# Performance work log

Hardware: AMD Instinct MI355X
Metric: run time of the kernel (lower is better)

The kernel has to match this reference:

```python
import jax, jax.numpy as jnp
import numpy as np


def setup_inputs() -> dict:
    key = jax.random.key(0)
    k1, k2, k3, k4 = jax.random.split(key, 4)
    B, T, C, H = 8, 2048, 1024, 1024
    return {
        "x": jax.random.normal(k1, (B, T, C), dtype=jnp.float32),
        "Wk": jax.random.normal(k2, (H, C), dtype=jnp.float32),
        "Wq": jax.random.normal(k3, (H, C), dtype=jnp.float32),
        "Wv": jax.random.normal(k4, (H, C), dtype=jnp.float32),
    }


def reference(x, Wk, Wq, Wv):
    # x: [B, T, C]; Wk/Wq/Wv: [H, C] (torch Linear stores [fan_out, fan_in])
    B, T, C = x.shape
    k = jnp.einsum('btc,hc->bth', x, Wk)  # [B, T, H]
    q = jnp.einsum('btc,hc->bth', x, Wq)
    v = jnp.einsum('btc,hc->bth', x, Wv)
    # NOTE: source scales by n_embd (C) ** -0.5, not head_size
    wei = jnp.einsum('bth,bsh->bts', q, k) * (C ** -0.5)  # [B, T, T]
    causal = jnp.tril(jnp.ones((T, T), dtype=bool))
    wei = jnp.where(causal, wei, -jnp.inf)
    wei = jax.nn.softmax(wei, axis=-1)
    # Dropout omitted (inference behavior; p=0.5 train-only in source)
    out = jnp.einsum('bts,bsh->bth', wei, v)  # [B, T, H]
    return (out, wei)
```

## Files before the change

kernel.cpp:

```cpp
#include <hip/hip_runtime.h>
#include <hip/hip_bf16.h>


#define BB 8
#define TT 2048
#define CC 1024
#define HH 1024
#define BT (BB * TT)

typedef _Float16 f16x8 __attribute__((ext_vector_type(8)));
typedef _Float16 f16x4 __attribute__((ext_vector_type(4)));
typedef float f32x4 __attribute__((ext_vector_type(4)));

#define AS1 __attribute__((address_space(1)))
#define AS3 __attribute__((address_space(3)))

__device__ __forceinline__ void gld16(const _Float16* g, _Float16* lds) {
    __builtin_amdgcn_global_load_lds((AS1 const unsigned int*)g,
                                     (AS3 unsigned int*)lds, 16, 0, 0);
}

__global__ __launch_bounds__(256) void split_kernel(
    const float* __restrict__ src, _Float16* __restrict__ dh,
    _Float16* __restrict__ dl, int n)
{
    int i = (blockIdx.x * 256 + threadIdx.x) * 4;
    if (i >= n) return;
    float4 v = *(const float4*)(src + i);
    f16x4 h, l;
    h[0] = (_Float16)v.x; l[0] = (_Float16)(v.x - (float)h[0]);
    h[1] = (_Float16)v.y; l[1] = (_Float16)(v.y - (float)h[1]);
    h[2] = (_Float16)v.z; l[2] = (_Float16)(v.z - (float)h[2]);
    h[3] = (_Float16)v.w; l[3] = (_Float16)(v.w - (float)h[3]);
    *(f16x4*)&dh[i] = h;
    *(f16x4*)&dl[i] = l;
}

__global__ __launch_bounds__(256) void splitT_kernel(
    const float* __restrict__ W, _Float16* __restrict__ th,
    _Float16* __restrict__ tl)
{
    __shared__ float L[64][65];
    const int h0 = blockIdx.x * 64;
    const int c0 = blockIdx.y * 64;
    const int tid = threadIdx.x;
    {
        const int hl = tid >> 2;
        const int cs = (tid & 3) * 16;
#pragma unroll
        for (int jj = 0; jj < 16; jj += 4) {
            float4 v = *(const float4*)&W[(size_t)(h0 + hl) * CC + c0 + cs + jj];
            L[cs + jj + 0][hl] = v.x;
            L[cs + jj + 1][hl] = v.y;
            L[cs + jj + 2][hl] = v.z;
            L[cs + jj + 3][hl] = v.w;
        }
    }
    __syncthreads();
    const int c  = tid >> 2;
    const int hs = (tid & 3) * 16;
    f16x8 hv0, hv1, lv0, lv1;
#pragma unroll
    for (int i = 0; i < 8; ++i) {
        float a = L[c][hs + i], b = L[c][hs + 8 + i];
        hv0[i] = (_Float16)a; lv0[i] = (_Float16)(a - (float)hv0[i]);
        hv1[i] = (_Float16)b; lv1[i] = (_Float16)(b - (float)hv1[i]);
    }
    size_t o = (size_t)(c0 + c) * HH + h0 + hs;
    *(f16x8*)&th[o] = hv0; *(f16x8*)&th[o + 8] = hv1;
    *(f16x8*)&tl[o] = lv0; *(f16x8*)&tl[o + 8] = lv1;
}

__global__ __launch_bounds__(256, 2) void mm_kernel(
    const _Float16* __restrict__ aH, const _Float16* __restrict__ aL,
    const _Float16* __restrict__ bH, const _Float16* __restrict__ bL,
    _Float16* __restrict__ mtH, _Float16* __restrict__ mtL)
{
    __shared__ _Float16 Ah[4096], Al[4096], Bh[4096], Bl[4096];

    const int n0 = blockIdx.x * 128;
    const int m0 = blockIdx.y * 128;

    const int tid  = threadIdx.x;
    const int r0   = tid & 127;
    const int k0   = tid >> 7;
    const int wave = tid >> 6;
    const int lane = tid & 63;
    const int quad = lane >> 4;
    const int lrow = lane & 15;
    const int wr   = (wave >> 1) * 64;
    const int wc   = (wave & 1) * 64;

    const size_t ga = (size_t)(m0 + r0) * HH + k0 * 8;
    const size_t gb = (size_t)(n0 + r0) * HH + k0 * 8;
    const int lds0 = tid * 8, lds1 = (tid + 256) * 8;

    f32x4 acc[4][4] = {};

    for (int kc = 0; kc < HH; kc += 32) {
        __syncthreads();
        gld16(aH + ga + kc,      &Ah[lds0]);
        gld16(aH + ga + kc + 16, &Ah[lds1]);
        gld16(aL + ga + kc,      &Al[lds0]);
        gld16(aL + ga + kc + 16, &Al[lds1]);
        gld16(bH + gb + kc,      &Bh[lds0]);
        gld16(bH + gb + kc + 16, &Bh[lds1]);
        gld16(bL + gb + kc,      &Bl[lds0]);
        gld16(bL + gb + kc + 16, &Bl[lds1]);
        __syncthreads();

        f16x8 ahf[4], alf[4], bhf[4], blf[4];
#pragma unroll
        for (int i = 0; i < 4; ++i) {
            ahf[i] = *(const f16x8*)&Ah[(quad * 128 + wr + i * 16 + lrow) * 8];
            alf[i] = *(const f16x8*)&Al[(quad * 128 + wr + i * 16 + lrow) * 8];
            bhf[i] = *(const f16x8*)&Bh[(quad * 128 + wc + i * 16 + lrow) * 8];
            blf[i] = *(const f16x8*)&Bl[(quad * 128 + wc + i * 16 + lrow) * 8];
        }
#pragma unroll
        for (int i = 0; i < 4; ++i)
#pragma unroll
            for (int j = 0; j < 4; ++j) {
                acc[i][j] = __builtin_amdgcn_mfma_f32_16x16x32_f16(ahf[i], bhf[j], acc[i][j], 0, 0, 0);
                acc[i][j] = __builtin_amdgcn_mfma_f32_16x16x32_f16(ahf[i], blf[j], acc[i][j], 0, 0, 0);
                acc[i][j] = __builtin_amdgcn_mfma_f32_16x16x32_f16(alf[i], bhf[j], acc[i][j], 0, 0, 0);
            }
    }

#pragma unroll
    for (int i = 0; i < 4; ++i)
#pragma unroll
        for (int j = 0; j < 4; ++j) {
            int mm = m0 + wr + i * 16 + quad * 4;
            int nn = n0 + wc + j * 16 + lrow;
            f16x4 ph, pl;
#pragma unroll
            for (int r = 0; r < 4; ++r) {
                float val = acc[i][j][r];
                _Float16 h = (_Float16)val;
                ph[r] = h;
                pl[r] = (_Float16)(val - (float)h);
            }
            *(f16x4*)&mtH[(size_t)nn * CC + mm] = ph;
            *(f16x4*)&mtL[(size_t)nn * CC + mm] = pl;
        }
}

#define EPI_STRIDE 136
__global__ __launch_bounds__(256, 2) void pv_kernel(
    const _Float16* __restrict__ xh, const _Float16* __restrict__ xl,
    const _Float16* __restrict__ mtH, const _Float16* __restrict__ mtL,
    const _Float16* __restrict__ Wvh,
    _Float16* __restrict__ Ph, _Float16* __restrict__ Pl,
    _Float16* __restrict__ vT)
{
    __shared__ _Float16 S[24576];

    const int idx   = blockIdx.x;
    const int z     = idx >> 10;
    const int r     = idx & 1023;
    const int xcd   = r & 7;
    const int j7    = r >> 3;
    const int mtile = xcd * 16 + (j7 >> 3);
    const int ntile = j7 & 7;
    const int m0 = mtile * 128;
    const int n0 = ntile * 128;

    const int tid  = threadIdx.x;
    const int r0   = tid & 127;
    const int k0   = tid >> 7;
    const int wave = tid >> 6;
    const int lane = tid & 63;
    const int quad = lane >> 4;
    const int lrow = lane & 15;
    const int wr   = (wave >> 1) * 64;
    const int wc   = (wave & 1) * 64;

    const size_t ga = (size_t)(m0 + r0) * CC + k0 * 8;
    const int lds0 = tid * 8, lds1 = (tid + 256) * 8;

    f32x4 acc[4][4] = {};

    if (z == 0) {
#define PV_A(kc_, sp_) do { \
        _Float16* Sb = S + (sp_) * 8192; \
        gld16(xh + ga + (kc_),      &Sb[lds0]); \
        gld16(xh + ga + (kc_) + 16, &Sb[lds1]); \
        gld16(xl + ga + (kc_),      &Sb[4096 + lds0]); \
        gld16(xl + ga + (kc_) + 16, &Sb[4096 + lds1]); \
    } while (0)
        PV_A(0, 0);
        PV_A(32, 1);
        int sa = 0;
        for (int kc = 0; kc < CC; kc += 32) {
            asm volatile("s_waitcnt vmcnt(4)" ::: "memory");
            __builtin_amdgcn_s_barrier();
            __builtin_amdgcn_sched_barrier(0);

            f16x8 bhf[4], blf[4];
#pragma unroll
            for (int j = 0; j < 4; ++j) {
                const size_t gbj = (size_t)(n0 + wc + j * 16 + lrow) * CC + kc + quad * 8;
                bhf[j] = *(const f16x8*)&mtH[gbj];
                blf[j] = *(const f16x8*)&mtL[gbj];
            }
            __builtin_amdgcn_sched_barrier(0);

            int ka = kc + 64; if (ka > CC - 32) ka = CC - 32;
            int s2 = sa + 2; if (s2 >= 3) s2 -= 3;
            PV_A(ka, s2);
            __builtin_amdgcn_sched_barrier(0);

            const _Float16* Ah = S + sa * 8192;
            const _Float16* Al = Ah + 4096;
            f16x8 ahf[4], alf[4];
#pragma unroll
            for (int i = 0; i < 4; ++i) {
                ahf[i] = *(const f16x8*)&Ah[(quad * 128 + wr + i * 16 + lrow) * 8];
                alf[i] = *(const f16x8*)&Al[(quad * 128 + wr + i * 16 + lrow) * 8];
            }
            __builtin_amdgcn_s_setprio(1);
#pragma unroll
            for (int i = 0; i < 4; ++i)
#pragma unroll
                for (int j = 0; j < 4; ++j) {
                    acc[i][j] = __builtin_amdgcn_mfma_f32_16x16x32_f16(ahf[i], bhf[j], acc[i][j], 0, 0, 0);
                    acc[i][j] = __builtin_amdgcn_mfma_f32_16x16x32_f16(ahf[i], blf[j], acc[i][j], 0, 0, 0);
                    acc[i][j] = __builtin_amdgcn_mfma_f32_16x16x32_f16(alf[i], bhf[j], acc[i][j], 0, 0, 0);
                }
            __builtin_amdgcn_s_setprio(0);

            ++sa; if (sa == 3) sa = 0;
        }
    } else {
#define PV_S1(kc_, sp_) do { \
        _Float16* Sb = S + (sp_) * 4096; \
        gld16(xh + ga + (kc_),      &Sb[lds0]); \
        gld16(xh + ga + (kc_) + 16, &Sb[lds1]); \
    } while (0)
        PV_S1(0, 0);
        PV_S1(32, 1);
        int sl = 0;
        for (int kc = 0; kc < CC; kc += 32) {
            asm volatile("s_waitcnt vmcnt(2)" ::: "memory");
            __builtin_amdgcn_s_barrier();
            __builtin_amdgcn_sched_barrier(0);

            f16x8 bhf[4];
#pragma unroll
            for (int j = 0; j < 4; ++j) {
                const size_t gbj = (size_t)(n0 + wc + j * 16 + lrow) * CC + kc + quad * 8;
                bhf[j] = *(const f16x8*)&Wvh[gbj];
            }
            __builtin_amdgcn_sched_barrier(0);

            int ka = kc + 64; if (ka > CC - 32) ka = CC - 32;
            int s2 = sl + 2; if (s2 >= 3) s2 -= 3;
            PV_S1(ka, s2);
            __builtin_amdgcn_sched_barrier(0);

            const _Float16* Ah = S + sl * 4096;
            f16x8 ahf[4];
#pragma unroll
            for (int i = 0; i < 4; ++i)
                ahf[i] = *(const f16x8*)&Ah[(quad * 128 + wr + i * 16 + lrow) * 8];
            __builtin_amdgcn_s_setprio(1);
#pragma unroll
            for (int i = 0; i < 4; ++i)
#pragma unroll
                for (int j = 0; j < 4; ++j)
                    acc[i][j] = __builtin_amdgcn_mfma_f32_16x16x32_f16(ahf[i], bhf[j], acc[i][j], 0, 0, 0);
            __builtin_amdgcn_s_setprio(0);

            ++sl; if (sl == 3) sl = 0;
        }
    }

    asm volatile("s_waitcnt vmcnt(0)" ::: "memory");
    __syncthreads();

    if (z == 1) {
#pragma unroll
        for (int i = 0; i < 4; ++i)
#pragma unroll
            for (int j = 0; j < 4; ++j) {
                int hl = wc + j * 16 + lrow;
                int tl = wr + i * 16 + quad * 4;
                f16x4 p;
#pragma unroll
                for (int rr = 0; rr < 4; ++rr) p[rr] = (_Float16)acc[i][j][rr];
                *(f16x4*)&S[hl * EPI_STRIDE + tl] = p;
            }
        __syncthreads();
        const int bi  = mtile >> 4;
        const int t0g = (mtile & 15) * 128;
        _Float16* vb = vT + (size_t)bi * HH * TT;
#pragma unroll
        for (int rr = 0; rr < 128; rr += 16) {
            int h = rr + (tid >> 4);
            int t = (tid & 15) * 8;
            f16x8 val = *(const f16x8*)&S[h * EPI_STRIDE + t];
            *(f16x8*)&vb[(size_t)(n0 + h) * TT + t0g + t] = val;
        }
    } else {
#pragma unroll
        for (int i = 0; i < 4; ++i)
#pragma unroll
            for (int j = 0; j < 4; ++j) {
                int tl = wr + i * 16 + quad * 4;
                int cl = wc + j * 16 + lrow;
#pragma unroll
                for (int rr = 0; rr < 4; ++rr)
                    S[(tl + rr) * EPI_STRIDE + cl] = (_Float16)acc[i][j][rr];
            }
        __syncthreads();
#pragma unroll
        for (int rr = 0; rr < 128; rr += 16) {
            int t = rr + (tid >> 4);
            int c = (tid & 15) * 8;
            f16x8 val = *(const f16x8*)&S[t * EPI_STRIDE + c];
            *(f16x8*)&Ph[(size_t)(m0 + t) * CC + n0 + c] = val;
        }
        __syncthreads();
#pragma unroll
        for (int i = 0; i < 4; ++i)
#pragma unroll
            for (int j = 0; j < 4; ++j) {
                int tl = wr + i * 16 + quad * 4;
                int cl = wc + j * 16 + lrow;
#pragma unroll
                for (int rr = 0; rr < 4; ++rr) {
                    float val = acc[i][j][rr];
                    _Float16 h = (_Float16)val;
                    S[(tl + rr) * EPI_STRIDE + cl] = (_Float16)(val - (float)h);
                }
            }
        __syncthreads();
#pragma unroll
        for (int rr = 0; rr < 128; rr += 16) {
            int t = rr + (tid >> 4);
            int c = (tid & 15) * 8;
            f16x8 val = *(const f16x8*)&S[t * EPI_STRIDE + c];
            *(f16x8*)&Pl[(size_t)(m0 + t) * CC + n0 + c] = val;
        }
    }
}

__global__ __launch_bounds__(256, 2) void logits_kernel(
    const _Float16* __restrict__ Ph, const _Float16* __restrict__ Pl,
    const _Float16* __restrict__ xh, const _Float16* __restrict__ xl,
    float* __restrict__ wei)
{
    __shared__ _Float16 S[24576];

    const int id  = blockIdx.x;
    const int b   = id & 7;
    const int tri = id >> 3;
    int tt = (int)((sqrtf(8.0f * (float)tri + 1.0f) - 1.0f) * 0.5f);
    while ((tt + 1) * (tt + 2) / 2 <= tri) ++tt;
    while (tt * (tt + 1) / 2 > tri) --tt;
    const int st = tri - tt * (tt + 1) / 2;

    const size_t base = (size_t)b * TT * CC;
    float* wb = wei + (size_t)b * TT * TT;
    const int m0 = tt * 128;
    const int n0 = st * 128;

    const int tid  = threadIdx.x;
    const int r0   = tid & 127;
    const int k0   = tid >> 7;
    const int wave = tid >> 6;
    const int lane = tid & 63;
    const int quad = lane >> 4;
    const int lrow = lane & 15;
    const int wr   = (wave >> 1) * 64;
    const int wc   = (wave & 1) * 64;

    const size_t ga = base + (size_t)(m0 + r0) * CC + k0 * 8;
    const _Float16* xhb = xh + base;
    const _Float16* xlb = xl + base;
    const int lds0 = tid * 8, lds1 = (tid + 256) * 8;

    f32x4 acc[4][4] = {};

#define LG_A(kc_, sp_) do { \
    _Float16* Sb = S + (sp_) * 8192; \
    gld16(Ph + ga + (kc_),      &Sb[lds0]); \
    gld16(Ph + ga + (kc_) + 16, &Sb[lds1]); \
    gld16(Pl + ga + (kc_),      &Sb[4096 + lds0]); \
    gld16(Pl + ga + (kc_) + 16, &Sb[4096 + lds1]); \
} while (0)

    LG_A(0, 0);
    LG_A(32, 1);

    int sa = 0;
    for (int kc = 0; kc < CC; kc += 32) {
        asm volatile("s_waitcnt vmcnt(4)" ::: "memory");
        __builtin_amdgcn_s_barrier();
        __builtin_amdgcn_sched_barrier(0);

        f16x8 bhf[4], blf[4];
#pragma unroll
        for (int j = 0; j < 4; ++j) {
            const size_t gbj = (size_t)(n0 + wc + j * 16 + lrow) * CC + kc + quad * 8;
            bhf[j] = *(const f16x8*)&xhb[gbj];
            blf[j] = *(const f16x8*)&xlb[gbj];
        }
        __builtin_amdgcn_sched_barrier(0);

        int ka = kc + 64; if (ka > CC - 32) ka = CC - 32;
        int s2 = sa + 2; if (s2 >= 3) s2 -= 3;
        LG_A(ka, s2);
        __builtin_amdgcn_sched_barrier(0);

        const _Float16* Ah = S + sa * 8192;
        const _Float16* Al = Ah + 4096;
        f16x8 ahf[4], alf[4];
#pragma unroll
        for (int i = 0; i < 4; ++i) {
            ahf[i] = *(const f16x8*)&Ah[(quad * 128 + wr + i * 16 + lrow) * 8];
            alf[i] = *(const f16x8*)&Al[(quad * 128 + wr + i * 16 + lrow) * 8];
        }
        __builtin_amdgcn_s_setprio(1);
#pragma unroll
        for (int i = 0; i < 4; ++i)
#pragma unroll
            for (int j = 0; j < 4; ++j) {
                acc[i][j] = __builtin_amdgcn_mfma_f32_16x16x32_f16(ahf[i], bhf[j], acc[i][j], 0, 0, 0);
                acc[i][j] = __builtin_amdgcn_mfma_f32_16x16x32_f16(ahf[i], blf[j], acc[i][j], 0, 0, 0);
                acc[i][j] = __builtin_amdgcn_mfma_f32_16x16x32_f16(alf[i], bhf[j], acc[i][j], 0, 0, 0);
            }
        __builtin_amdgcn_s_setprio(0);

        ++sa; if (sa == 3) sa = 0;
    }

    asm volatile("s_waitcnt vmcnt(0)" ::: "memory");

    const float scale = 0.03125f;
#pragma unroll
    for (int i = 0; i < 4; ++i)
#pragma unroll
        for (int j = 0; j < 4; ++j)
#pragma unroll
            for (int r = 0; r < 4; ++r) {
                int rr = wr + i * 16 + quad * 4 + r;
                int cc = wc + j * 16 + lrow;
                wb[(size_t)(m0 + rr) * TT + n0 + cc] = acc[i][j][r] * scale;
            }
}

__global__ __launch_bounds__(256) void softmax_kernel(
    float* __restrict__ wei, _Float16* __restrict__ wei16)
{
    const int t = blockIdx.x;
    const int b = blockIdx.y;
    float* row = wei + (size_t)b * TT * TT + (size_t)t * TT;
    _Float16* row16 = wei16 + (size_t)b * TT * TT + (size_t)t * TT;
    const int n = t + 1;
    const int tid = threadIdx.x;
    const int base = tid * 8;

    float vals[8];
    if (base < n) {
        float4 v0 = *(const float4*)&row[base];
        float4 v1 = *(const float4*)&row[base + 4];
        vals[0] = v0.x; vals[1] = v0.y; vals[2] = v0.z; vals[3] = v0.w;
        vals[4] = v1.x; vals[5] = v1.y; vals[6] = v1.z; vals[7] = v1.w;
    } else {
#pragma unroll
        for (int i = 0; i < 8; ++i) vals[i] = -INFINITY;
    }

    float mx = -INFINITY;
#pragma unroll
    for (int i = 0; i < 8; ++i) {
        if (base + i >= n) vals[i] = -INFINITY;
        mx = fmaxf(mx, vals[i]);
    }
#pragma unroll
    for (int off = 32; off > 0; off >>= 1)
        mx = fmaxf(mx, __shfl_down(mx, off));

    __shared__ float redm[4];
    __shared__ float reds[4];
    if ((tid & 63) == 0) redm[tid >> 6] = mx;
    __syncthreads();
    const float m = fmaxf(fmaxf(redm[0], redm[1]), fmaxf(redm[2], redm[3]));

    float sum = 0.f;
#pragma unroll
    for (int i = 0; i < 8; ++i) {
        vals[i] = __expf(vals[i] - m);
        sum += vals[i];
    }
#pragma unroll
    for (int off = 32; off > 0; off >>= 1)
        sum += __shfl_down(sum, off);
    if ((tid & 63) == 0) reds[tid >> 6] = sum;
    __syncthreads();
    const float inv = 1.0f / (reds[0] + reds[1] + reds[2] + reds[3]);

    f16x8 h;
#pragma unroll
    for (int i = 0; i < 8; ++i) {
        float w = vals[i] * inv;
        vals[i] = w;
        h[i] = (_Float16)w;
    }
    *(float4*)&row[base]     = make_float4(vals[0], vals[1], vals[2], vals[3]);
    *(float4*)&row[base + 4] = make_float4(vals[4], vals[5], vals[6], vals[7]);
    *(f16x8*)&row16[base]    = h;
}

__global__ __launch_bounds__(256, 3) void out_kernel(
    const _Float16* __restrict__ wei16, const _Float16* __restrict__ vT,
    float* __restrict__ out)
{
    __shared__ _Float16 S[12288];

    const int id = blockIdx.x;
    const int b  = id & 7;
    const int r  = id >> 3;
    const int tt = 15 - (r >> 3);
    const int nb = r & 7;

    const _Float16* wb = wei16 + (size_t)b * TT * TT;
    const _Float16* vb = vT    + (size_t)b * HH * TT;
    float*          ob = out   + (size_t)b * TT * HH;

    const int m0 = tt * 128;
    const int n0 = nb * 128;
    const int kend = (tt + 1) * 128;

    const int tid  = threadIdx.x;
    const int r0   = tid & 127;
    const int k0   = tid >> 7;
    const int wave = tid >> 6;
    const int lane = tid & 63;
    const int quad = lane >> 4;
    const int lrow = lane & 15;
    const int wr   = (wave >> 1) * 64;
    const int wc   = (wave & 1) * 64;

    const size_t ga = (size_t)(m0 + r0) * TT + k0 * 8;
    const int lds0 = tid * 8, lds1 = (tid + 256) * 8;

    f32x4 acc[4][4] = {};

#define OUT_A(kc_, sp_) do { \
    _Float16* Sb = S + (sp_) * 4096; \
    gld16(wb + ga + (kc_),      &Sb[lds0]); \
    gld16(wb + ga + (kc_) + 16, &Sb[lds1]); \
} while (0)

    OUT_A(0, 0);
    OUT_A(32, 1);

    int sl = 0;
    for (int kc = 0; kc < kend; kc += 32) {
        asm volatile("s_waitcnt vmcnt(2)" ::: "memory");
        __builtin_amdgcn_s_barrier();
        __builtin_amdgcn_sched_barrier(0);

        f16x8 bhf[4];
#pragma unroll
        for (int j = 0; j < 4; ++j) {
            const size_t gbj = (size_t)(n0 + wc + j * 16 + lrow) * TT + kc + quad * 8;
            bhf[j] = *(const f16x8*)&vb[gbj];
        }
        __builtin_amdgcn_sched_barrier(0);

        int ka = kc + 64; if (ka > kend - 32) ka = kend - 32;
        int s2 = sl + 2; if (s2 >= 3) s2 -= 3;
        OUT_A(ka, s2);
        __builtin_amdgcn_sched_barrier(0);

        const _Float16* Ah = S + sl * 4096;
        f16x8 ahf[4];
#pragma unroll
        for (int i = 0; i < 4; ++i)
            ahf[i] = *(const f16x8*)&Ah[(quad * 128 + wr + i * 16 + lrow) * 8];
        __builtin_amdgcn_s_setprio(1);
#pragma unroll
        for (int i = 0; i < 4; ++i)
#pragma unroll
            for (int j = 0; j < 4; ++j)
                acc[i][j] = __builtin_amdgcn_mfma_f32_16x16x32_f16(ahf[i], bhf[j], acc[i][j], 0, 0, 0);
        __builtin_amdgcn_s_setprio(0);

        ++sl; if (sl == 3) sl = 0;
    }

    asm volatile("s_waitcnt vmcnt(0)" ::: "memory");

#pragma unroll
    for (int i = 0; i < 4; ++i)
#pragma unroll
        for (int j = 0; j < 4; ++j)
#pragma unroll
            for (int r2 = 0; r2 < 4; ++r2) {
                int rr = wr + i * 16 + quad * 4 + r2;
                int cc = wc + j * 16 + lrow;
                ob[(size_t)(m0 + rr) * HH + n0 + cc] = acc[i][j][r2];
            }
}

extern "C" void kernel_launch(void* const* d_in, const int* in_sizes, int n_in,
                              void* d_out, int out_size, void* d_ws, size_t ws_size,
                              hipStream_t stream)
{
    const float* x  = (const float*)d_in[0];
    const float* Wk = (const float*)d_in[1];
    const float* Wq = (const float*)d_in[2];
    const float* Wv = (const float*)d_in[3];

    const size_t NX = (size_t)BT * CC;
    const size_t NW = (size_t)HH * CC;

    float* out = (float*)d_out;
    float* wei = out + (size_t)BT * HH;

    _Float16* WqTh = (_Float16*)out;
    _Float16* WqTl = WqTh + NW;
    _Float16* WkTh = WqTl + NW;
    _Float16* WkTl = WkTh + NW;
    _Float16* Wvh  = WkTl + NW;
    _Float16* Wvl  = Wvh  + NW;
    _Float16* MTh  = Wvl  + NW;
    _Float16* MTl  = MTh  + NW;

    _Float16* xh = (_Float16*)d_ws;
    _Float16* xl = xh + NX;
    _Float16* Ph = xl + NX;
    _Float16* Pl = Ph + NX;
    _Float16* vT = Pl + NX;
    _Float16* wei16 = (_Float16*)d_ws;

    split_kernel<<<dim3(NX / 1024), 256, 0, stream>>>(x, xh, xl, (int)NX);
    splitT_kernel<<<dim3(HH / 64, CC / 64), 256, 0, stream>>>(Wq, WqTh, WqTl);
    splitT_kernel<<<dim3(HH / 64, CC / 64), 256, 0, stream>>>(Wk, WkTh, WkTl);
    split_kernel<<<dim3(NW / 1024), 256, 0, stream>>>(Wv, Wvh, Wvl, (int)NW);

    mm_kernel<<<dim3(CC / 128, CC / 128), 256, 0, stream>>>(
        WqTh, WqTl, WkTh, WkTl, MTh, MTl);
    pv_kernel<<<dim3(2048), 256, 0, stream>>>(
        xh, xl, MTh, MTl, Wvh, Ph, Pl, vT);
    logits_kernel<<<dim3(136 * BB), 256, 0, stream>>>(
        Ph, Pl, xh, xl, wei);
    softmax_kernel<<<dim3(TT, BB), 256, 0, stream>>>(wei, wei16);
    out_kernel<<<dim3(128 * BB), 256, 0, stream>>>(wei16, vT, out);
}
```

Baseline: 967.3 us.

## Prefetch B-operand register fragments one k-step ahead in the GEMM loops

The three MFMA GEMM loops (projection, QK^T logits, and PV output) now load the next k-slice's B-operand fragments from global memory into a second register set while the current slice is computed. The loop is unrolled by two to ping-pong between the two register sets. This hides global-load latency that was previously exposed right after the barrier. In exchange it uses more VGPRs, drops the s_setprio hints, and assumes the output loop's k extent is a multiple of 64.

```diff
diff --git a/kernel.cpp b/kernel.cpp
--- a/kernel.cpp
+++ b/kernel.cpp
@@ -189,90 +189,105 @@
         gld16(xl + ga + (kc_),      &Sb[4096 + lds0]); \
         gld16(xl + ga + (kc_) + 16, &Sb[4096 + lds1]); \
     } while (0)
+
+#define PV_ITER0(kc_, BHC, BLC, BHN, BLN) do { \
+        asm volatile("s_waitcnt vmcnt(4)" ::: "memory"); \
+        __builtin_amdgcn_s_barrier(); \
+        __builtin_amdgcn_sched_barrier(0); \
+        { int kb = (kc_) + 32; if (kb > CC - 32) kb = CC - 32; \
+          _Pragma("unroll") \
+          for (int j = 0; j < 4; ++j) { \
+              const size_t gbj = (size_t)(n0 + wc + j * 16 + lrow) * CC + kb + quad * 8; \
+              BHN[j] = *(const f16x8*)&mtH[gbj]; \
+              BLN[j] = *(const f16x8*)&mtL[gbj]; \
+          } } \
+        __builtin_amdgcn_sched_barrier(0); \
+        { int ka = (kc_) + 64; if (ka > CC - 32) ka = CC - 32; \
+          int s2 = sa + 2; if (s2 >= 3) s2 -= 3; \
+          PV_A(ka, s2); } \
+        __builtin_amdgcn_sched_barrier(0); \
+        { const _Float16* Ah = S + sa * 8192; \
+          const _Float16* Al = Ah + 4096; \
+          f16x8 ahf[4], alf[4]; \
+          _Pragma("unroll") \
+          for (int i = 0; i < 4; ++i) { \
+              ahf[i] = *(const f16x8*)&Ah[(quad * 128 + wr + i * 16 + lrow) * 8]; \
+              alf[i] = *(const f16x8*)&Al[(quad * 128 + wr + i * 16 + lrow) * 8]; \
+          } \
+          _Pragma("unroll") \
+          for (int i = 0; i < 4; ++i) \
+              _Pragma("unroll") \
+              for (int j = 0; j < 4; ++j) { \
+                  acc[i][j] = __builtin_amdgcn_mfma_f32_16x16x32_f16(ahf[i], BHC[j], acc[i][j], 0, 0, 0); \
+                  acc[i][j] = __builtin_amdgcn_mfma_f32_16x16x32_f16(ahf[i], BLC[j], acc[i][j], 0, 0, 0); \
+                  acc[i][j] = __builtin_amdgcn_mfma_f32_16x16x32_f16(alf[i], BHC[j], acc[i][j], 0, 0, 0); \
+              } } \
+        ++sa; if (sa == 3) sa = 0; \
+    } while (0)
+
+        f16x8 bhA[4], blA[4], bhB[4], blB[4];
+#pragma unroll
+        for (int j = 0; j < 4; ++j) {
+            const size_t gbj = (size_t)(n0 + wc + j * 16 + lrow) * CC + quad * 8;
+            bhA[j] = *(const f16x8*)&mtH[gbj];
+            blA[j] = *(const f16x8*)&mtL[gbj];
+        }
+        __builtin_amdgcn_sched_barrier(0);
         PV_A(0, 0);
         PV_A(32, 1);
         int sa = 0;
-        for (int kc = 0; kc < CC; kc += 32) {
-            asm volatile("s_waitcnt vmcnt(4)" ::: "memory");
-            __builtin_amdgcn_s_barrier();
-            __builtin_amdgcn_sched_barrier(0);
-
-            f16x8 bhf[4], blf[4];
-#pragma unroll
-            for (int j = 0; j < 4; ++j) {
-                const size_t gbj = (size_t)(n0 + wc + j * 16 + lrow) * CC + kc + quad * 8;
-                bhf[j] = *(const f16x8*)&mtH[gbj];
-                blf[j] = *(const f16x8*)&mtL[gbj];
-            }
-            __builtin_amdgcn_sched_barrier(0);
-
-            int ka = kc + 64; if (ka > CC - 32) ka = CC - 32;
-            int s2 = sa + 2; if (s2 >= 3) s2 -= 3;
-            PV_A(ka, s2);
-            __builtin_amdgcn_sched_barrier(0);
-
-            const _Float16* Ah = S + sa * 8192;
-            const _Float16* Al = Ah + 4096;
-            f16x8 ahf[4], alf[4];
-#pragma unroll
-            for (int i = 0; i < 4; ++i) {
-                ahf[i] = *(const f16x8*)&Ah[(quad * 128 + wr + i * 16 + lrow) * 8];
-                alf[i] = *(const f16x8*)&Al[(quad * 128 + wr + i * 16 + lrow) * 8];
-            }
-            __builtin_amdgcn_s_setprio(1);
-#pragma unroll
-            for (int i = 0; i < 4; ++i)
-#pragma unroll
-                for (int j = 0; j < 4; ++j) {
-                    acc[i][j] = __builtin_amdgcn_mfma_f32_16x16x32_f16(ahf[i], bhf[j], acc[i][j], 0, 0, 0);
-                    acc[i][j] = __builtin_amdgcn_mfma_f32_16x16x32_f16(ahf[i], blf[j], acc[i][j], 0, 0, 0);
-                    acc[i][j] = __builtin_amdgcn_mfma_f32_16x16x32_f16(alf[i], bhf[j], acc[i][j], 0, 0, 0);
-                }
-            __builtin_amdgcn_s_setprio(0);
-
-            ++sa; if (sa == 3) sa = 0;
+        for (int kc = 0; kc < CC; kc += 64) {
+            PV_ITER0(kc,      bhA, blA, bhB, blB);
+            PV_ITER0(kc + 32, bhB, blB, bhA, blA);
         }
     } else {
-#define PV_S1(kc_, sp_) do { \
+#define PV_A1(kc_, sp_) do { \
         _Float16* Sb = S + (sp_) * 4096; \
         gld16(xh + ga + (kc_),      &Sb[lds0]); \
         gld16(xh + ga + (kc_) + 16, &Sb[lds1]); \
     } while (0)
-        PV_S1(0, 0);
-        PV_S1(32, 1);
+
+#define PV_ITER1(kc_, BHC, BHN) do { \
+        asm volatile("s_waitcnt vmcnt(2)" ::: "memory"); \
+        __builtin_amdgcn_s_barrier(); \
+        __builtin_amdgcn_sched_barrier(0); \
+        { int kb = (kc_) + 32; if (kb > CC - 32) kb = CC - 32; \
+          _Pragma("unroll") \
+          for (int j = 0; j < 4; ++j) { \
+              const size_t gbj = (size_t)(n0 + wc + j * 16 + lrow) * CC + kb + quad * 8; \
+              BHN[j] = *(const f16x8*)&Wvh[gbj]; \
+          } } \
+        __builtin_amdgcn_sched_barrier(0); \
+        { int ka = (kc_) + 64; if (ka > CC - 32) ka = CC - 32; \
+          int s2 = sl + 2; if (s2 >= 3) s2 -= 3; \
+          PV_A1(ka, s2); } \
+        __builtin_amdgcn_sched_barrier(0); \
+        { const _Float16* Ah = S + sl * 4096; \
+          f16x8 ahf[4]; \
+          _Pragma("unroll") \
+          for (int i = 0; i < 4; ++i) \
+              ahf[i] = *(const f16x8*)&Ah[(quad * 128 + wr + i * 16 + lrow) * 8]; \
+          _Pragma("unroll") \
+          for (int i = 0; i < 4; ++i) \
+              _Pragma("unroll") \
+              for (int j = 0; j < 4; ++j) \
+                  acc[i][j] = __builtin_amdgcn_mfma_f32_16x16x32_f16(ahf[i], BHC[j], acc[i][j], 0, 0, 0); } \
+        ++sl; if (sl == 3) sl = 0; \
+    } while (0)
+
+        f16x8 bhA[4], bhB[4];
+#pragma unroll
+        for (int j = 0; j < 4; ++j) {
+            const size_t gbj = (size_t)(n0 + wc + j * 16 + lrow) * CC + quad * 8;
+            bhA[j] = *(const f16x8*)&Wvh[gbj];
+        }
+        __builtin_amdgcn_sched_barrier(0);
+        PV_A1(0, 0);
+        PV_A1(32, 1);
         int sl = 0;
-        for (int kc = 0; kc < CC; kc += 32) {
-            asm volatile("s_waitcnt vmcnt(2)" ::: "memory");
-            __builtin_amdgcn_s_barrier();
-            __builtin_amdgcn_sched_barrier(0);
-
-            f16x8 bhf[4];
-#pragma unroll
-            for (int j = 0; j < 4; ++j) {
-                const size_t gbj = (size_t)(n0 + wc + j * 16 + lrow) * CC + kc + quad * 8;
-                bhf[j] = *(const f16x8*)&Wvh[gbj];
-            }
-            __builtin_amdgcn_sched_barrier(0);
-
-            int ka = kc + 64; if (ka > CC - 32) ka = CC - 32;
-            int s2 = sl + 2; if (s2 >= 3) s2 -= 3;
-            PV_S1(ka, s2);
-            __builtin_amdgcn_sched_barrier(0);
-
-            const _Float16* Ah = S + sl * 4096;
-            f16x8 ahf[4];
-#pragma unroll
-            for (int i = 0; i < 4; ++i)
-                ahf[i] = *(const f16x8*)&Ah[(quad * 128 + wr + i * 16 + lrow) * 8];
-            __builtin_amdgcn_s_setprio(1);
-#pragma unroll
-            for (int i = 0; i < 4; ++i)
-#pragma unroll
-                for (int j = 0; j < 4; ++j)
-                    acc[i][j] = __builtin_amdgcn_mfma_f32_16x16x32_f16(ahf[i], bhf[j], acc[i][j], 0, 0, 0);
-            __builtin_amdgcn_s_setprio(0);
-
-            ++sl; if (sl == 3) sl = 0;
+        for (int kc = 0; kc < CC; kc += 64) {
+            PV_ITER1(kc,      bhA, bhB);
+            PV_ITER1(kc + 32, bhB, bhA);
         }
     }
 
@@ -391,49 +406,55 @@
     gld16(Pl + ga + (kc_) + 16, &Sb[4096 + lds1]); \
 } while (0)
 
+#define LG_ITER(kc_, BHC, BLC, BHN, BLN) do { \
+    asm volatile("s_waitcnt vmcnt(4)" ::: "memory"); \
+    __builtin_amdgcn_s_barrier(); \
+    __builtin_amdgcn_sched_barrier(0); \
+    { int kb = (kc_) + 32; if (kb > CC - 32) kb = CC - 32; \
+      _Pragma("unroll") \
+      for (int j = 0; j < 4; ++j) { \
+          const size_t gbj = (size_t)(n0 + wc + j * 16 + lrow) * CC + kb + quad * 8; \
+          BHN[j] = *(const f16x8*)&xhb[gbj]; \
+          BLN[j] = *(const f16x8*)&xlb[gbj]; \
+      } } \
+    __builtin_amdgcn_sched_barrier(0); \
+    { int ka = (kc_) + 64; if (ka > CC - 32) ka = CC - 32; \
+      int s2 = sa + 2; if (s2 >= 3) s2 -= 3; \
+      LG_A(ka, s2); } \
+    __builtin_amdgcn_sched_barrier(0); \
+    { const _Float16* Ah = S + sa * 8192; \
+      const _Float16* Al = Ah + 4096; \
+      f16x8 ahf[4], alf[4]; \
+      _Pragma("unroll") \
+      for (int i = 0; i < 4; ++i) { \
+          ahf[i] = *(const f16x8*)&Ah[(quad * 128 + wr + i * 16 + lrow) * 8]; \
+          alf[i] = *(const f16x8*)&Al[(quad * 128 + wr + i * 16 + lrow) * 8]; \
+      } \
+      _Pragma("unroll") \
+      for (int i = 0; i < 4; ++i) \
+          _Pragma("unroll") \
+          for (int j = 0; j < 4; ++j) { \
+              acc[i][j] = __builtin_amdgcn_mfma_f32_16x16x32_f16(ahf[i], BHC[j], acc[i][j], 0, 0, 0); \
+              acc[i][j] = __builtin_amdgcn_mfma_f32_16x16x32_f16(ahf[i], BLC[j], acc[i][j], 0, 0, 0); \
+              acc[i][j] = __builtin_amdgcn_mfma_f32_16x16x32_f16(alf[i], BHC[j], acc[i][j], 0, 0, 0); \
+          } } \
+    ++sa; if (sa == 3) sa = 0; \
+} while (0)
+
+    f16x8 bhA[4], blA[4], bhB[4], blB[4];
+#pragma unroll
+    for (int j = 0; j < 4; ++j) {
+        const size_t gbj = (size_t)(n0 + wc + j * 16 + lrow) * CC + quad * 8;
+        bhA[j] = *(const f16x8*)&xhb[gbj];
+        blA[j] = *(const f16x8*)&xlb[gbj];
+    }
+    __builtin_amdgcn_sched_barrier(0);
     LG_A(0, 0);
     LG_A(32, 1);
-
     int sa = 0;
-    for (int kc = 0; kc < CC; kc += 32) {
-        asm volatile("s_waitcnt vmcnt(4)" ::: "memory");
-        __builtin_amdgcn_s_barrier();
-        __builtin_amdgcn_sched_barrier(0);
-
-        f16x8 bhf[4], blf[4];
-#pragma unroll
-        for (int j = 0; j < 4; ++j) {
-            const size_t gbj = (size_t)(n0 + wc + j * 16 + lrow) * CC + kc + quad * 8;
-            bhf[j] = *(const f16x8*)&xhb[gbj];
-            blf[j] = *(const f16x8*)&xlb[gbj];
-        }
-        __builtin_amdgcn_sched_barrier(0);
-
-        int ka = kc + 64; if (ka > CC - 32) ka = CC - 32;
-        int s2 = sa + 2; if (s2 >= 3) s2 -= 3;
-        LG_A(ka, s2);
-        __builtin_amdgcn_sched_barrier(0);
-
-        const _Float16* Ah = S + sa * 8192;
-        const _Float16* Al = Ah + 4096;
-        f16x8 ahf[4], alf[4];
-#pragma unroll
-        for (int i = 0; i < 4; ++i) {
-            ahf[i] = *(const f16x8*)&Ah[(quad * 128 + wr + i * 16 + lrow) * 8];
-            alf[i] = *(const f16x8*)&Al[(quad * 128 + wr + i * 16 + lrow) * 8];
-        }
-        __builtin_amdgcn_s_setprio(1);
-#pragma unroll
-        for (int i = 0; i < 4; ++i)
-#pragma unroll
-            for (int j = 0; j < 4; ++j) {
-                acc[i][j] = __builtin_amdgcn_mfma_f32_16x16x32_f16(ahf[i], bhf[j], acc[i][j], 0, 0, 0);
-                acc[i][j] = __builtin_amdgcn_mfma_f32_16x16x32_f16(ahf[i], blf[j], acc[i][j], 0, 0, 0);
-                acc[i][j] = __builtin_amdgcn_mfma_f32_16x16x32_f16(alf[i], bhf[j], acc[i][j], 0, 0, 0);
-            }
-        __builtin_amdgcn_s_setprio(0);
-
-        ++sa; if (sa == 3) sa = 0;
+    for (int kc = 0; kc < CC; kc += 64) {
+        LG_ITER(kc,      bhA, blA, bhB, blB);
+        LG_ITER(kc + 32, bhB, blB, bhA, blA);
     }
 
     asm volatile("s_waitcnt vmcnt(0)" ::: "memory");
@@ -555,42 +576,45 @@
     gld16(wb + ga + (kc_) + 16, &Sb[lds1]); \
 } while (0)
 
+#define OUT_ITER(kc_, BHC, BHN) do { \
+    asm volatile("s_waitcnt vmcnt(2)" ::: "memory"); \
+    __builtin_amdgcn_s_barrier(); \
+    __builtin_amdgcn_sched_barrier(0); \
+    { int kb = (kc_) + 32; if (kb > kend - 32) kb = kend - 32; \
+      _Pragma("unroll") \
+      for (int j = 0; j < 4; ++j) { \
+          const size_t gbj = (size_t)(n0 + wc + j * 16 + lrow) * TT + kb + quad * 8; \
+          BHN[j] = *(const f16x8*)&vb[gbj]; \
+      } } \
+    __builtin_amdgcn_sched_barrier(0); \
+    { int ka = (kc_) + 64; if (ka > kend - 32) ka = kend - 32; \
+      int s2 = sl + 2; if (s2 >= 3) s2 -= 3; \
+      OUT_A(ka, s2); } \
+    __builtin_amdgcn_sched_barrier(0); \
+    { const _Float16* Ah = S + sl * 4096; \
+      f16x8 ahf[4]; \
+      _Pragma("unroll") \
+      for (int i = 0; i < 4; ++i) \
+          ahf[i] = *(const f16x8*)&Ah[(quad * 128 + wr + i * 16 + lrow) * 8]; \
+      _Pragma("unroll") \
+      for (int i = 0; i < 4; ++i) \
+          _Pragma("unroll") \
+          for (int j = 0; j < 4; ++j) \
+              acc[i][j] = __builtin_amdgcn_mfma_f32_16x16x32_f16(ahf[i], BHC[j], acc[i][j], 0, 0, 0); } \
+    ++sl; if (sl == 3) sl = 0; \
+} while (0)
+
+    f16x8 bvA[4], bvB[4];
+#pragma unroll
+    for (int j = 0; j < 4; ++j)
+        bvA[j] = *(const f16x8*)&vb[(size_t)(n0 + wc + j * 16 + lrow) * TT + quad * 8];
+    __builtin_amdgcn_sched_barrier(0);
     OUT_A(0, 0);
     OUT_A(32, 1);
-
     int sl = 0;
-    for (int kc = 0; kc < kend; kc += 32) {
-        asm volatile("s_waitcnt vmcnt(2)" ::: "memory");
-        __builtin_amdgcn_s_barrier();
-        __builtin_amdgcn_sched_barrier(0);
-
-        f16x8 bhf[4];
-#pragma unroll
-        for (int j = 0; j < 4; ++j) {
-            const size_t gbj = (size_t)(n0 + wc + j * 16 + lrow) * TT + kc + quad * 8;
-            bhf[j] = *(const f16x8*)&vb[gbj];
-        }
-        __builtin_amdgcn_sched_barrier(0);
-
-        int ka = kc + 64; if (ka > kend - 32) ka = kend - 32;
-        int s2 = sl + 2; if (s2 >= 3) s2 -= 3;
-        OUT_A(ka, s2);
-        __builtin_amdgcn_sched_barrier(0);
-
-        const _Float16* Ah = S + sl * 4096;
-        f16x8 ahf[4];
-#pragma unroll
-        for (int i = 0; i < 4; ++i)
-            ahf[i] = *(const f16x8*)&Ah[(quad * 128 + wr + i * 16 + lrow) * 8];
-        __builtin_amdgcn_s_setprio(1);
-#pragma unroll
-        for (int i = 0; i < 4; ++i)
-#pragma unroll
-            for (int j = 0; j < 4; ++j)
-                acc[i][j] = __builtin_amdgcn_mfma_f32_16x16x32_f16(ahf[i], bhf[j], acc[i][j], 0, 0, 0);
-        __builtin_amdgcn_s_setprio(0);
-
-        ++sl; if (sl == 3) sl = 0;
+    for (int kc = 0; kc < kend; kc += 64) {
+        OUT_ITER(kc,      bvA, bvB);
+        OUT_ITER(kc + 32, bvB, bvA);
     }
 
     asm volatile("s_waitcnt vmcnt(0)" ::: "memory");
```

Measured after the change: 973.5 us. Within noise of the previous version (+0.6%).
